# Kernel tuning notes

Measured on AMD Instinct MI355X. Metric: run time of the kernel, lower is better.

## Reference

```python
import jax, jax.numpy as jnp
import numpy as np

F_SIZE = 1024
N_HEADS = 16
HEAD = F_SIZE // N_HEADS
EPS = 1e-5


def setup_inputs() -> dict:
    key = jax.random.key(0)
    ks = jax.random.split(key, 8)
    B, N, F = 4, 1024, F_SIZE
    in_feats = jax.random.normal(ks[0], (B, N, F), dtype=jnp.float32)
    pos_feats = jax.random.normal(ks[1], (B, N, F), dtype=jnp.float32)
    # parameters (torch Linear convention: W [out, in], y = x @ W.T + b)
    xav = lambda k, o, i: jax.random.uniform(k, (o, i), jnp.float32, -1.0, 1.0) * np.sqrt(6.0 / (o + i))
    ln_g = jnp.ones((F,), jnp.float32)
    ln_b = jnp.zeros((F,), jnp.float32)
    w_qk = xav(ks[2], 2 * F, F)
    b_qk = jnp.zeros((2 * F,), jnp.float32)
    w_v = xav(ks[3], F, F)
    b_v = jnp.zeros((F,), jnp.float32)
    w_o = xav(ks[4], F, F)
    b_o = jnp.zeros((F,), jnp.float32)
    return {"in_feats": in_feats, "pos_feats": pos_feats, "ln_g": ln_g, "ln_b": ln_b,
            "w_qk": w_qk, "b_qk": b_qk, "w_v": w_v, "b_v": b_v, "w_o": w_o, "b_o": b_o}


def reference(in_feats, pos_feats, ln_g, ln_b, w_qk, b_qk, w_v, b_v, w_o, b_o):
    B, N, F = in_feats.shape
    H, D = N_HEADS, HEAD
    # LayerNorm (biased variance, eps=1e-5 as torch default)
    mu = jnp.mean(in_feats, axis=-1, keepdims=True)
    var = jnp.mean(jnp.square(in_feats - mu), axis=-1, keepdims=True)
    norm = (in_feats - mu) * jax.lax.rsqrt(var + EPS) * ln_g + ln_b
    pos_norm = norm + pos_feats
    # QK projection on pos-added features, V projection on norm features
    qk = pos_norm @ w_qk.T + b_qk                      # [B,N,2F]
    q = qk[..., :F].reshape(B, N, H, D)
    k = qk[..., F:].reshape(B, N, H, D)
    v = (norm @ w_v.T + b_v).reshape(B, N, H, D)
    scale = float(D) ** -0.5
    scores = jnp.einsum('bnhd,bmhd->bhnm', q, k) * scale
    attn = jax.nn.softmax(scores, axis=-1)
    wv = jnp.einsum('bhnm,bmhd->bnhd', attn, v).reshape(B, N, F)
    delta = wv @ w_o.T + b_o
    return in_feats + delta
```

## Files before the change

### kernel.cpp

```cpp
#include <hip/hip_runtime.h>
#include <hip/hip_bf16.h>
#include <stdint.h>

#define FDIM 1024
#define NHEADS 16
#define HDIM 64
#define BATCH 4
#define SEQ 1024
#define MROWS (BATCH*SEQ)

typedef short bf16x8 __attribute__((ext_vector_type(8)));
typedef float f32x4 __attribute__((ext_vector_type(4)));

__device__ inline unsigned short f2bf(float f){
  union { float f; uint32_t u; } v; v.f = f;
  uint32_t u = v.u;
  uint32_t r = (u + 0x7fffu + ((u >> 16) & 1u)) >> 16;
  return (unsigned short)r;
}

__device__ inline void gld_lds16(const void* g, void* l){
  __builtin_amdgcn_global_load_lds((const __attribute__((address_space(1))) uint32_t*)g,
                                   (__attribute__((address_space(3))) uint32_t*)l, 16, 0, 0);
}

__device__ inline bf16x8 ldsw(const unsigned short* base, int row, int colgrp){
  return *(const bf16x8*)&base[row*64 + (((colgrp) ^ (row&7))<<3)];
}

template<int N>
__device__ inline float dppRor(float x){
  int r = __builtin_amdgcn_update_dpp(0, __float_as_int(x), 0x120|N, 0xF, 0xF, true);
  return __int_as_float(r);
}
__device__ inline float rowMax16(float x){
  x = fmaxf(x, dppRor<1>(x)); x = fmaxf(x, dppRor<2>(x));
  x = fmaxf(x, dppRor<4>(x)); x = fmaxf(x, dppRor<8>(x));
  return x;
}
__device__ inline float rowSum16(float x){
  x += dppRor<1>(x); x += dppRor<2>(x); x += dppRor<4>(x); x += dppRor<8>(x);
  return x;
}

__global__ __launch_bounds__(256) void cvt_all(const float* __restrict__ wqk,
                                               const float* __restrict__ wv,
                                               const float* __restrict__ wo,
                                               unsigned short* __restrict__ oqk,
                                               unsigned short* __restrict__ ov,
                                               unsigned short* __restrict__ oo){
  int i = blockIdx.x*256 + threadIdx.x;
  const float* src; unsigned short* dst; int j;
  if (i < 524288)      { src = wqk; dst = oqk; j = i; }
  else if (i < 786432) { src = wv;  dst = ov;  j = i - 524288; }
  else                 { src = wo;  dst = oo;  j = i - 786432; }
  float4 v = ((const float4*)src)[j];
  ushort4 o; o.x=f2bf(v.x); o.y=f2bf(v.y); o.z=f2bf(v.z); o.w=f2bf(v.w);
  ((ushort4*)dst)[j] = o;
}

__global__ __launch_bounds__(256) void ln_posadd(const float* __restrict__ x,
                                                 const float* __restrict__ pos,
                                                 const float* __restrict__ g,
                                                 const float* __restrict__ be,
                                                 unsigned short* __restrict__ normb,
                                                 unsigned short* __restrict__ posnb){
  int row = blockIdx.x, t = threadIdx.x;
  float4 v = ((const float4*)(x + (size_t)row*FDIM))[t];
  float s  = v.x+v.y+v.z+v.w;
  float sq = v.x*v.x+v.y*v.y+v.z*v.z+v.w*v.w;
  #pragma unroll
  for (int off=32; off>=1; off>>=1){ s += __shfl_down(s,off); sq += __shfl_down(sq,off); }
  __shared__ float red[8];
  int w=t>>6, lane=t&63;
  if (!lane){ red[w]=s; red[4+w]=sq; }
  __syncthreads();
  s  = red[0]+red[1]+red[2]+red[3];
  sq = red[4]+red[5]+red[6]+red[7];
  float mu  = s*(1.0f/FDIM);
  float var = sq*(1.0f/FDIM) - mu*mu;
  float rs  = rsqrtf(var + 1e-5f);
  float4 gg=((const float4*)g)[t], bb=((const float4*)be)[t];
  float4 pp=((const float4*)(pos + (size_t)row*FDIM))[t];
  float n0=(v.x-mu)*rs*gg.x+bb.x, n1=(v.y-mu)*rs*gg.y+bb.y;
  float n2=(v.z-mu)*rs*gg.z+bb.z, n3=(v.w-mu)*rs*gg.w+bb.w;
  ushort4 nb; nb.x=f2bf(n0); nb.y=f2bf(n1); nb.z=f2bf(n2); nb.w=f2bf(n3);
  ushort4 pb; pb.x=f2bf(n0+pp.x); pb.y=f2bf(n1+pp.y); pb.z=f2bf(n2+pp.z); pb.w=f2bf(n3+pp.w);
  ((ushort4*)(normb+(size_t)row*FDIM))[t]=nb;
  ((ushort4*)(posnb+(size_t)row*FDIM))[t]=pb;
}

#define QSCL 0.1803368801111204f
template<int MODE>
__global__ __launch_bounds__(256) void gemm_bt(const unsigned short* __restrict__ A,
                                               const unsigned short* __restrict__ Bw,
                                               const float* __restrict__ bias,
                                               const float* __restrict__ resid,
                                               void* __restrict__ Cout,
                                               int M, int Nout, int K){
  __shared__ unsigned short Als[128*32];
  __shared__ unsigned short Bls[128*32];
  int t = threadIdx.x, w = t>>6, lane = t&63;
  int m0 = blockIdx.x*128, n0 = blockIdx.y*128;
  int wm = (w>>1)*64, wn = (w&1)*64;
  int lrow = lane&15, lk = (lane>>4)*8, rg = lane>>4;
  f32x4 acc[4][4] = {};
  for (int k0=0; k0<K; k0+=32){
    #pragma unroll
    for (int i=0;i<2;i++){
      int c = t + i*256;
      gld_lds16(A  + (size_t)(m0 + (c>>2))*K + k0 + (c&3)*8, Als + c*8);
      gld_lds16(Bw + (size_t)(n0 + (c>>2))*K + k0 + (c&3)*8, Bls + c*8);
    }
    __syncthreads();
    bf16x8 a[4], b[4];
    #pragma unroll
    for (int i=0;i<4;i++){
      a[i] = *(const bf16x8*)&Als[(wm + i*16 + lrow)*32 + lk];
      b[i] = *(const bf16x8*)&Bls[(wn + i*16 + lrow)*32 + lk];
    }
    #pragma unroll
    for (int mi=0;mi<4;mi++)
      #pragma unroll
      for (int ni=0;ni<4;ni++)
        acc[mi][ni] = __builtin_amdgcn_mfma_f32_16x16x32_bf16(a[mi], b[ni], acc[mi][ni], 0,0,0);
    __syncthreads();
  }
  #pragma unroll
  for (int mi=0;mi<4;mi++){
    #pragma unroll
    for (int ni=0;ni<4;ni++){
      int n = n0 + wn + ni*16 + lrow;
      float bs = (MODE==2) ? 0.f : bias[n];
      float scl = (MODE==3 && n < FDIM) ? QSCL : 1.0f;
      #pragma unroll
      for (int r=0;r<4;r++){
        int m = m0 + wm + mi*16 + rg*4 + r;
        float vv = acc[mi][ni][r] + ((MODE==2) ? bias[m] : bs);
        if (MODE==3) vv *= scl;
        size_t idx = (size_t)m*Nout + n;
        if (MODE==1) ((float*)Cout)[idx] = vv + resid[idx];
        else         ((unsigned short*)Cout)[idx] = f2bf(vv);
      }
    }
  }
}

__global__ __launch_bounds__(256, 4) void attn(const unsigned short* __restrict__ qk,
                                               const unsigned short* __restrict__ vt,
                                               unsigned short* __restrict__ wvbuf){
  __shared__ unsigned short Pls[64*64];
  int t=threadIdx.x, w=t>>6, lane=t&63;
  int lrow=lane&15, lcg=lane>>4, rg=lane>>4;
  int bid = blockIdx.x;
  int wgid = (bid&7)*128 + (bid>>3);
  int q0 = (wgid&15)*64, h = (wgid>>4)&15, b = wgid>>8;
  const size_t qs = 2*FDIM;

  const unsigned short* qrow = qk + (size_t)(b*SEQ + q0 + w*16 + lrow)*qs + h*HDIM;
  bf16x8 qa0 = *(const bf16x8*)(qrow + lcg*8);
  bf16x8 qa1 = *(const bf16x8*)(qrow + 32 + lcg*8);

  const unsigned short* kbase = qk + (size_t)(b*SEQ + lrow)*qs + FDIM + h*HDIM + lcg*8;
  const unsigned short* vbase = vt + (size_t)(h*HDIM + lrow)*MROWS + b*SEQ + lcg*8;

  f32x4 o[4] = {};
  float m_run[4], l_run[4];
  #pragma unroll
  for (int r=0;r<4;r++){ m_run[r]=-1e30f; l_run[r]=0.f; }

  for (int kt=0; kt<16; ++kt){
    f32x4 s[4] = {};
    #pragma unroll
    for (int ni=0;ni<4;ni++){
      bf16x8 kb0 = *(const bf16x8*)(kbase + (size_t)(kt*64 + ni*16)*qs);
      bf16x8 kb1 = *(const bf16x8*)(kbase + (size_t)(kt*64 + ni*16)*qs + 32);
      s[ni] = __builtin_amdgcn_mfma_f32_16x16x32_bf16(qa0, kb0, s[ni], 0,0,0);
      s[ni] = __builtin_amdgcn_mfma_f32_16x16x32_bf16(qa1, kb1, s[ni], 0,0,0);
    }
    #pragma unroll
    for (int r=0;r<4;r++){
      float tm = fmaxf(fmaxf(s[0][r],s[1][r]), fmaxf(s[2][r],s[3][r]));
      tm = rowMax16(tm);
      float mn = fmaxf(m_run[r], tm);
      float sc = exp2f(m_run[r] - mn);
      float p[4]; float ts = 0.f;
      #pragma unroll
      for (int ni=0;ni<4;ni++){ p[ni] = exp2f(s[ni][r] - mn); ts += p[ni]; }
      ts = rowSum16(ts);
      l_run[r] = l_run[r]*sc + ts;
      m_run[r] = mn;
      #pragma unroll
      for (int nd=0;nd<4;nd++) o[nd][r] *= sc;
      int pr = w*16 + rg*4 + r;
      #pragma unroll
      for (int ni=0;ni<4;ni++)
        Pls[pr*64 + (((ni*2 + (lrow>>3)) ^ (pr&7))<<3) + (lrow&7)] = f2bf(p[ni]);
    }
    #pragma unroll
    for (int kf=0; kf<2; kf++){
      bf16x8 pa = ldsw(Pls, w*16+lrow, kf*4 + lcg);
      #pragma unroll
      for (int nd=0;nd<4;nd++){
        bf16x8 vb = *(const bf16x8*)(vbase + (size_t)(nd*16)*MROWS + kt*64 + kf*32);
        o[nd] = __builtin_amdgcn_mfma_f32_16x16x32_bf16(pa, vb, o[nd], 0,0,0);
      }
    }
  }
  #pragma unroll
  for (int nd=0; nd<4; nd++){
    #pragma unroll
    for (int r=0;r<4;r++){
      float val = o[nd][r] / l_run[r];
      wvbuf[(size_t)(b*SEQ + q0 + w*16 + rg*4 + r)*FDIM + h*HDIM + nd*16 + lrow] = f2bf(val);
    }
  }
}

extern "C" void kernel_launch(void* const* d_in, const int* in_sizes, int n_in,
                              void* d_out, int out_size, void* d_ws, size_t ws_size,
                              hipStream_t stream) {
  const float* in_feats = (const float*)d_in[0];
  const float* pos      = (const float*)d_in[1];
  const float* ln_g     = (const float*)d_in[2];
  const float* ln_b     = (const float*)d_in[3];
  const float* w_qk     = (const float*)d_in[4];
  const float* b_qk     = (const float*)d_in[5];
  const float* w_v      = (const float*)d_in[6];
  const float* b_v      = (const float*)d_in[7];
  const float* w_o      = (const float*)d_in[8];
  const float* b_o      = (const float*)d_in[9];
  float* out = (float*)d_out;

  char* ws = (char*)d_ws;
  unsigned short* norm_b = (unsigned short*)(ws + 0);
  unsigned short* posn_b = (unsigned short*)(ws + (8u<<20));
  unsigned short* wqk_b  = (unsigned short*)(ws + (16u<<20));
  unsigned short* wv_b   = (unsigned short*)(ws + (20u<<20));
  unsigned short* wo_b   = (unsigned short*)(ws + (22u<<20));
  unsigned short* qk_buf = (unsigned short*)(ws + (24u<<20));
  unsigned short* vt_buf = (unsigned short*)(ws + (40u<<20));
  unsigned short* wv_out = norm_b;

  cvt_all<<<4096, 256, 0, stream>>>(w_qk, w_v, w_o, wqk_b, wv_b, wo_b);
  ln_posadd<<<MROWS, 256, 0, stream>>>(in_feats, pos, ln_g, ln_b, norm_b, posn_b);
  gemm_bt<3><<<dim3(MROWS/128, 2048/128), 256, 0, stream>>>(posn_b, wqk_b, b_qk, nullptr,
                                                            qk_buf, MROWS, 2048, FDIM);
  gemm_bt<2><<<dim3(FDIM/128, MROWS/128), 256, 0, stream>>>(wv_b, norm_b, b_v, nullptr,
                                                            vt_buf, FDIM, MROWS, FDIM);
  attn<<<dim3(SEQ/64 * NHEADS * BATCH), 256, 0, stream>>>(qk_buf, vt_buf, wv_out);
  gemm_bt<1><<<dim3(MROWS/128, 1024/128), 256, 0, stream>>>(wv_out, wo_b, b_o, in_feats,
                                                            out, MROWS, 1024, FDIM);
}
```

Baseline: 305.2 us.

## Rewrite attention with 32x32 MFMA, S-transposed register softmax, and lazy rescaling

Each wave now handles 32 query rows and computes S^T = K·Q^T with 32x32x16 MFMAs, so every lane holds one query column and the row max and sum need only a single cross-half shuffle instead of DPP reductions. The P tile is packed to bf16 with v_cvt_pk and permuted between the two lane halves so it can feed the PV MFMA directly, which removes the LDS round trip and its shared memory. The output is rescaled only when the running max grows by more than a threshold, and K/V fragments are double-buffered in registers across 32-key subtiles. The grid shrinks to 512 blocks of 128 queries and launch bounds drop to 2 waves, which raises register pressure and lowers occupancy.

```diff
diff --git a/kernel.cpp b/kernel.cpp
--- a/kernel.cpp
+++ b/kernel.cpp
@@ -11,6 +11,7 @@
 
 typedef short bf16x8 __attribute__((ext_vector_type(8)));
 typedef float f32x4 __attribute__((ext_vector_type(4)));
+typedef float f32x16 __attribute__((ext_vector_type(16)));
 
 __device__ inline unsigned short f2bf(float f){
   union { float f; uint32_t u; } v; v.f = f;
@@ -19,28 +20,15 @@
   return (unsigned short)r;
 }
 
+__device__ inline uint32_t cvtpk(float lo, float hi){
+  uint32_t r;
+  asm("v_cvt_pk_bf16_f32 %0, %1, %2" : "=v"(r) : "v"(lo), "v"(hi));
+  return r;
+}
+
 __device__ inline void gld_lds16(const void* g, void* l){
   __builtin_amdgcn_global_load_lds((const __attribute__((address_space(1))) uint32_t*)g,
                                    (__attribute__((address_space(3))) uint32_t*)l, 16, 0, 0);
-}
-
-__device__ inline bf16x8 ldsw(const unsigned short* base, int row, int colgrp){
-  return *(const bf16x8*)&base[row*64 + (((colgrp) ^ (row&7))<<3)];
-}
-
-template<int N>
-__device__ inline float dppRor(float x){
-  int r = __builtin_amdgcn_update_dpp(0, __float_as_int(x), 0x120|N, 0xF, 0xF, true);
-  return __int_as_float(r);
-}
-__device__ inline float rowMax16(float x){
-  x = fmaxf(x, dppRor<1>(x)); x = fmaxf(x, dppRor<2>(x));
-  x = fmaxf(x, dppRor<4>(x)); x = fmaxf(x, dppRor<8>(x));
-  return x;
-}
-__device__ inline float rowSum16(float x){
-  x += dppRor<1>(x); x += dppRor<2>(x); x += dppRor<4>(x); x += dppRor<8>(x);
-  return x;
 }
 
 __global__ __launch_bounds__(256) void cvt_all(const float* __restrict__ wqk,
@@ -146,74 +134,101 @@
   }
 }
 
-__global__ __launch_bounds__(256, 4) void attn(const unsigned short* __restrict__ qk,
+__global__ __launch_bounds__(256, 2) void attn(const unsigned short* __restrict__ qk,
                                                const unsigned short* __restrict__ vt,
                                                unsigned short* __restrict__ wvbuf){
-  __shared__ unsigned short Pls[64*64];
   int t=threadIdx.x, w=t>>6, lane=t&63;
-  int lrow=lane&15, lcg=lane>>4, rg=lane>>4;
+  int q=lane&31, hi=lane>>5;
   int bid = blockIdx.x;
-  int wgid = (bid&7)*128 + (bid>>3);
-  int q0 = (wgid&15)*64, h = (wgid>>4)&15, b = wgid>>8;
+  int wgid = (bid&7)*64 + (bid>>3);
+  int qt = wgid&7, h = (wgid>>3)&15, b = wgid>>7;
+  int q0 = qt*128 + w*32;
   const size_t qs = 2*FDIM;
 
-  const unsigned short* qrow = qk + (size_t)(b*SEQ + q0 + w*16 + lrow)*qs + h*HDIM;
-  bf16x8 qa0 = *(const bf16x8*)(qrow + lcg*8);
-  bf16x8 qa1 = *(const bf16x8*)(qrow + 32 + lcg*8);
-
-  const unsigned short* kbase = qk + (size_t)(b*SEQ + lrow)*qs + FDIM + h*HDIM + lcg*8;
-  const unsigned short* vbase = vt + (size_t)(h*HDIM + lrow)*MROWS + b*SEQ + lcg*8;
-
-  f32x4 o[4] = {};
-  float m_run[4], l_run[4];
-  #pragma unroll
-  for (int r=0;r<4;r++){ m_run[r]=-1e30f; l_run[r]=0.f; }
-
-  for (int kt=0; kt<16; ++kt){
-    f32x4 s[4] = {};
-    #pragma unroll
-    for (int ni=0;ni<4;ni++){
-      bf16x8 kb0 = *(const bf16x8*)(kbase + (size_t)(kt*64 + ni*16)*qs);
-      bf16x8 kb1 = *(const bf16x8*)(kbase + (size_t)(kt*64 + ni*16)*qs + 32);
-      s[ni] = __builtin_amdgcn_mfma_f32_16x16x32_bf16(qa0, kb0, s[ni], 0,0,0);
-      s[ni] = __builtin_amdgcn_mfma_f32_16x16x32_bf16(qa1, kb1, s[ni], 0,0,0);
-    }
-    #pragma unroll
-    for (int r=0;r<4;r++){
-      float tm = fmaxf(fmaxf(s[0][r],s[1][r]), fmaxf(s[2][r],s[3][r]));
-      tm = rowMax16(tm);
-      float mn = fmaxf(m_run[r], tm);
-      float sc = exp2f(m_run[r] - mn);
-      float p[4]; float ts = 0.f;
-      #pragma unroll
-      for (int ni=0;ni<4;ni++){ p[ni] = exp2f(s[ni][r] - mn); ts += p[ni]; }
-      ts = rowSum16(ts);
-      l_run[r] = l_run[r]*sc + ts;
-      m_run[r] = mn;
-      #pragma unroll
-      for (int nd=0;nd<4;nd++) o[nd][r] *= sc;
-      int pr = w*16 + rg*4 + r;
-      #pragma unroll
-      for (int ni=0;ni<4;ni++)
-        Pls[pr*64 + (((ni*2 + (lrow>>3)) ^ (pr&7))<<3) + (lrow&7)] = f2bf(p[ni]);
-    }
-    #pragma unroll
-    for (int kf=0; kf<2; kf++){
-      bf16x8 pa = ldsw(Pls, w*16+lrow, kf*4 + lcg);
-      #pragma unroll
-      for (int nd=0;nd<4;nd++){
-        bf16x8 vb = *(const bf16x8*)(vbase + (size_t)(nd*16)*MROWS + kt*64 + kf*32);
-        o[nd] = __builtin_amdgcn_mfma_f32_16x16x32_bf16(pa, vb, o[nd], 0,0,0);
-      }
-    }
-  }
-  #pragma unroll
-  for (int nd=0; nd<4; nd++){
-    #pragma unroll
-    for (int r=0;r<4;r++){
-      float val = o[nd][r] / l_run[r];
-      wvbuf[(size_t)(b*SEQ + q0 + w*16 + rg*4 + r)*FDIM + h*HDIM + nd*16 + lrow] = f2bf(val);
-    }
+  const unsigned short* qptr = qk + (size_t)(b*SEQ + q0 + q)*qs + h*HDIM + hi*8;
+  bf16x8 qf[4];
+  #pragma unroll
+  for (int ks=0; ks<4; ks++) qf[ks] = *(const bf16x8*)(qptr + ks*16);
+
+  const unsigned short* kptr = qk + (size_t)(b*SEQ + q)*qs + FDIM + h*HDIM + hi*8;
+  const unsigned short* vptr = vt + (size_t)(h*HDIM + q)*MROWS + b*SEQ + hi*8;
+
+  f32x16 o0 = {}, o1 = {};
+  float m_run = -1e30f, l_run = 0.f;
+
+  bf16x8 kbA[4], vbA[2][2], kbB[4], vbB[2][2];
+
+  auto loadT = [&](bf16x8 (&kb)[4], bf16x8 (&vb)[2][2], int key0){
+    #pragma unroll
+    for (int ks=0; ks<4; ks++)
+      kb[ks] = *(const bf16x8*)(kptr + (size_t)key0*qs + ks*16);
+    #pragma unroll
+    for (int dt=0; dt<2; dt++)
+      #pragma unroll
+      for (int kp=0; kp<2; kp++)
+        vb[dt][kp] = *(const bf16x8*)(vptr + (size_t)dt*32*MROWS + key0 + kp*16);
+  };
+
+  auto body = [&](bf16x8 (&kb)[4], bf16x8 (&vb)[2][2]){
+    f32x16 s = {};
+    #pragma unroll
+    for (int ks=0; ks<4; ks++)
+      s = __builtin_amdgcn_mfma_f32_32x32x16_bf16(kb[ks], qf[ks], s, 0,0,0);
+    float tm = fmaxf(s[0], s[1]);
+    #pragma unroll
+    for (int r=2;r<16;r++) tm = fmaxf(tm, s[r]);
+    tm = fmaxf(tm, __shfl_xor(tm, 32));
+    if (!__all(tm <= m_run + 8.0f)){
+      float mn = fmaxf(m_run, tm);
+      float sc = exp2f(m_run - mn);
+      l_run *= sc;
+      #pragma unroll
+      for (int r=0;r<16;r++){ o0[r]*=sc; o1[r]*=sc; }
+      m_run = mn;
+    }
+    float p[16]; float ts = 0.f;
+    #pragma unroll
+    for (int r=0;r<16;r++){ p[r] = exp2f(s[r] - m_run); ts += p[r]; }
+    ts += __shfl_xor(ts, 32);
+    l_run += ts;
+    bf16x8 pf[2];
+    #pragma unroll
+    for (int kp=0; kp<2; kp++){
+      uint32_t w0 = cvtpk(p[8*kp+0], p[8*kp+1]);
+      uint32_t w1 = cvtpk(p[8*kp+2], p[8*kp+3]);
+      uint32_t w2 = cvtpk(p[8*kp+4], p[8*kp+5]);
+      uint32_t w3 = cvtpk(p[8*kp+6], p[8*kp+7]);
+      uint32_t e0 = __shfl_xor(hi ? w0 : w2, 32);
+      uint32_t e1 = __shfl_xor(hi ? w1 : w3, 32);
+      union { uint32_t u[4]; bf16x8 v; } fr;
+      fr.u[0] = hi ? e0 : w0;
+      fr.u[1] = hi ? e1 : w1;
+      fr.u[2] = hi ? w2 : e0;
+      fr.u[3] = hi ? w3 : e1;
+      pf[kp] = fr.v;
+    }
+    o0 = __builtin_amdgcn_mfma_f32_32x32x16_bf16(pf[0], vb[0][0], o0, 0,0,0);
+    o0 = __builtin_amdgcn_mfma_f32_32x32x16_bf16(pf[1], vb[0][1], o0, 0,0,0);
+    o1 = __builtin_amdgcn_mfma_f32_32x32x16_bf16(pf[0], vb[1][0], o1, 0,0,0);
+    o1 = __builtin_amdgcn_mfma_f32_32x32x16_bf16(pf[1], vb[1][1], o1, 0,0,0);
+  };
+
+  loadT(kbA, vbA, 0);
+  for (int it=0; it<16; ++it){
+    loadT(kbB, vbB, it*64 + 32);
+    body(kbA, vbA);
+    if (it < 15) loadT(kbA, vbA, it*64 + 64);
+    body(kbB, vbB);
+  }
+
+  #pragma unroll
+  for (int r=0;r<16;r++){
+    int qr = (r&3) + 8*(r>>2) + 4*hi;
+    float lq = __shfl(l_run, qr);
+    float inv = 1.0f / lq;
+    size_t base = (size_t)(b*SEQ + q0 + qr)*FDIM + h*HDIM + q;
+    wvbuf[base]      = f2bf(o0[r]*inv);
+    wvbuf[base + 32] = f2bf(o1[r]*inv);
   }
 }
 
@@ -248,7 +263,7 @@
                                                             qk_buf, MROWS, 2048, FDIM);
   gemm_bt<2><<<dim3(FDIM/128, MROWS/128), 256, 0, stream>>>(wv_b, norm_b, b_v, nullptr,
                                                             vt_buf, FDIM, MROWS, FDIM);
-  attn<<<dim3(SEQ/64 * NHEADS * BATCH), 256, 0, stream>>>(qk_buf, vt_buf, wv_out);
+  attn<<<dim3(512), 256, 0, stream>>>(qk_buf, vt_buf, wv_out);
   gemm_bt<1><<<dim3(MROWS/128, 1024/128), 256, 0, stream>>>(wv_out, wo_b, b_o, in_feats,
                                                             out, MROWS, 1024, FDIM);
 }
```

After: 250.9 us. 17.8% less time.
